# Kernel tuning notes

Hardware: AMD Instinct MI355X
Metric: run time of the kernel (lower is better)

## Reference

```python
import jax, jax.numpy as jnp
import numpy as np

IN_DIM = 128
OUT_DIM = 128
EDGE_DIM = 64
NUM_HEADS = 8
HEAD_DIM = OUT_DIM // NUM_HEADS
N_NODES = 10000
N_EDGES = 320000
LN_EPS = 1e-5


def _gelu(x):
    # torch nn.GELU default is the exact (erf) formulation
    return jax.nn.gelu(x, approximate=False)


def _layernorm(x, g, b):
    mu = jnp.mean(x, axis=-1, keepdims=True)
    var = jnp.var(x, axis=-1, keepdims=True)
    return (x - mu) * jax.lax.rsqrt(var + LN_EPS) * g + b


def setup_inputs() -> dict:
    key = jax.random.key(0)
    ks = jax.random.split(key, 16)

    def lin(k, fan_in, fan_out):
        # torch nn.Linear default init: U(-1/sqrt(fan_in), 1/sqrt(fan_in))
        bound = 1.0 / np.sqrt(fan_in)
        kw, kb = jax.random.split(k)
        w = jax.random.uniform(kw, (fan_in, fan_out), jnp.float32, -bound, bound)
        b = jax.random.uniform(kb, (fan_out,), jnp.float32, -bound, bound)
        return w, b

    node_features = jax.random.normal(ks[0], (N_NODES, IN_DIM), jnp.float32)
    edge_index = jax.random.randint(ks[1], (2, N_EDGES), 0, N_NODES)
    edge_attr = jax.random.normal(ks[2], (N_EDGES, EDGE_DIM), jnp.float32)

    msg_w1, msg_b1 = lin(ks[3], 2 * IN_DIM + EDGE_DIM, OUT_DIM)
    msg_w2, msg_b2 = lin(ks[4], OUT_DIM, OUT_DIM)
    q_w, q_b = lin(ks[5], IN_DIM, OUT_DIM)
    kv_w, kv_b = lin(ks[6], IN_DIM + EDGE_DIM, OUT_DIM)
    out_w1, out_b1 = lin(ks[7], IN_DIM + OUT_DIM, OUT_DIM)
    out_w2, out_b2 = lin(ks[8], OUT_DIM, OUT_DIM)
    ln_g = 1.0 + 0.02 * jax.random.normal(ks[9], (OUT_DIM,), jnp.float32)
    ln_b = 0.02 * jax.random.normal(ks[10], (OUT_DIM,), jnp.float32)

    return dict(node_features=node_features, edge_attr=edge_attr,
                msg_w1=msg_w1, msg_b1=msg_b1, msg_w2=msg_w2, msg_b2=msg_b2,
                q_w=q_w, q_b=q_b, kv_w=kv_w, kv_b=kv_b,
                out_w1=out_w1, out_b1=out_b1, out_w2=out_w2, out_b2=out_b2,
                ln_g=ln_g, ln_b=ln_b, edge_index=edge_index)


def reference(node_features, edge_attr, msg_w1, msg_b1, msg_w2, msg_b2,
              q_w, q_b, kv_w, kv_b, out_w1, out_b1, out_w2, out_b2,
              ln_g, ln_b, edge_index):
    N = node_features.shape[0]
    E = edge_index.shape[1]
    src, dst = edge_index[0], edge_index[1]

    s = node_features[src]                      # [E, Din]
    d = node_features[dst]                      # [E, Din]

    # message MLP
    m_in = jnp.concatenate([s, d, edge_attr], axis=-1)          # [E, 2*Din+De]
    m = _gelu(m_in @ msg_w1 + msg_b1) @ msg_w2 + msg_b2         # [E, Dout]

    # per-edge attention logits
    q = (d @ q_w + q_b).reshape(E, NUM_HEADS, HEAD_DIM)
    kv_in = jnp.concatenate([s, edge_attr], axis=-1)
    kv = (kv_in @ kv_w + kv_b).reshape(E, NUM_HEADS, HEAD_DIM)
    attn = jnp.sum(q * kv, axis=-1) * (HEAD_DIM ** -0.5)        # [E, H]

    # Deterministic version: pick the edge with the largest index per dst node.
    last = jnp.full((N,), -1, dtype=jnp.int32).at[dst].max(
        jnp.arange(E, dtype=jnp.int32))                          # [N]
    attn_full = jnp.where(last[:, None] >= 0,
                          attn[jnp.maximum(last, 0)],
                          -jnp.inf)                              # [N, H]
    # softmax over the NODE axis (dim=0), exactly as the torch code does;
    # -inf rows contribute 0, so using N instead of dst.max()+1 is identical.
    attn_norm = jax.nn.softmax(attn_full, axis=0)[dst]           # [E, H]

    m = (m.reshape(E, NUM_HEADS, HEAD_DIM) * attn_norm[..., None]).reshape(E, OUT_DIM)

    # scatter-add aggregation
    agg = jax.ops.segment_sum(m, dst, num_segments=N)            # [N, Dout]

    h_in = jnp.concatenate([node_features, agg], axis=-1)        # [N, Din+Dout]
    h = _gelu(h_in @ out_w1 + out_b1) @ out_w2 + out_b2          # [N, Dout]

    # res_proj is Identity since in_dim == out_dim; dropout is eval-mode no-op
    return _layernorm(node_features + h, ln_g, ln_b)
```

## Files before the change

kernel.cpp:

```cpp
#include <hip/hip_runtime.h>
#include <hip/hip_bf16.h>

#define NN 10000
#define NE 320000

typedef __bf16 bf16x8 __attribute__((ext_vector_type(8)));
typedef float  f32x4  __attribute__((ext_vector_type(4)));

__device__ __forceinline__ float bf2f(ushort u){
  union { uint i; float f; } c; c.i = ((uint)u) << 16; return c.f;
}
__device__ __forceinline__ ushort f2bf(float f){
  union { float f; uint i; } c; c.f = f;
  uint x = c.i;
  return (ushort)((x + 0x7FFFu + ((x >> 16) & 1u)) >> 16);
}
__device__ __forceinline__ float gelu_erf(float x){
  return 0.5f * x * (1.0f + erff(x * 0.70710678118654752f));
}
__device__ __forceinline__ float gelu_tanh(float x){
  float y = 0.7978845608028654f * (x + 0.044715f * x * x * x);
  float e = __expf(2.f * y);
  float th = 1.f - 2.f / (e + 1.f);
  return 0.5f * x * (1.f + th);
}
__device__ __forceinline__ uint encf(float f){
  uint u = __float_as_uint(f);
  return (u & 0x80000000u) ? ~u : (u | 0x80000000u);
}
__device__ __forceinline__ float decf(uint u){
  return __uint_as_float((u & 0x80000000u) ? (u & 0x7FFFFFFFu) : ~u);
}
#define MFMA16(a,b,c) __builtin_amdgcn_mfma_f32_16x16x32_bf16((a),(b),(c),0,0,0)

__global__ void k_init(const uint* __restrict__ w, int* __restrict__ flag,
                       int* __restrict__ cnt, int* __restrict__ last,
                       uint* __restrict__ Menc, float* __restrict__ S){
  int t = threadIdx.x;
  if (blockIdx.x == 0){
    uint c = 0;
    for (int i = t; i < 4096; i += 256){
      uint v = w[i * 63];
      uint e = (v >> 7) & 0xFF;
      if (e >= 100 && e <= 140) c++;
    }
    __shared__ uint red[256];
    red[t] = c; __syncthreads();
    for (int s = 128; s > 0; s >>= 1){
      if (t < s) red[t] += red[t + s];
      __syncthreads();
    }
    if (t == 0) *flag = (red[0] < 2048) ? 1 : 0;
    return;
  }
  int idx = (blockIdx.x - 1) * 256 + t;
  if (idx < 10000) last[idx] = -1;
  else if (idx < 20000) cnt[idx - 10000] = 0;
  else if (idx < 20008) Menc[idx - 20000] = 0u;
  else if (idx < 20016) S[idx - 20008] = 0.f;
}

__global__ void k_prep(
    const void* NF0, const int* __restrict__ dstI,
    const void* w1, const void* w2, const void* qw, const void* kvw,
    const void* ow1, const void* ow2,
    const void* b1, const void* b2, const void* qb, const void* kvb,
    const void* ob1, const void* ob2, const void* lg, const void* lb,
    int* __restrict__ cnt, int* __restrict__ last,
    ushort* NFc, float* Gagg, ushort* SB, ushort* KVW2,
    ushort* W1aT, ushort* W1bT, ushort* W1cT, ushort* W2T, ushort* QT, ushort* KVT,
    ushort* O1aT, ushort* O1bT, ushort* O2T, const int* flag)
{
  int f = *flag;
  int idx = blockIdx.x * 256 + threadIdx.x;
  if (idx < NE){
    int d = dstI[idx];
    atomicAdd(&cnt[d], 1);
    atomicMax(&last[d], idx);
    return;
  }
  idx -= NE;
  if (idx < 320000){
    if (f){
      float4 v = ((const float4*)NF0)[idx];
      ushort4 o; o.x=f2bf(v.x); o.y=f2bf(v.y); o.z=f2bf(v.z); o.w=f2bf(v.w);
      ((ushort4*)NFc)[idx] = o;
    } else ((ushort4*)NFc)[idx] = ((const ushort4*)NF0)[idx];
    return;
  }
  idx -= 320000;
  if (idx < 320000){ float4 z = {0.f,0.f,0.f,0.f}; ((float4*)Gagg)[idx] = z; return; }
  idx -= 320000;
  if (idx < 1024){
    const void* ps[8] = {b1,b2,qb,kvb,ob1,ob2,lg,lb};
    const void* p = ps[idx >> 7]; int j = idx & 127;
    SB[idx] = f ? f2bf(((const float*)p)[j]) : ((const ushort*)p)[j];
    return;
  }
  idx -= 1024;
  if (idx < 8192){
    KVW2[idx] = f ? f2bf(((const float*)kvw)[16384 + idx]) : ((const ushort*)kvw)[16384 + idx];
    return;
  }
  idx -= 8192;
  if (idx < 16384){ int c=idx>>7,k=idx&127; W1aT[idx] = f? f2bf(((const float*)w1)[k*128+c]) : ((const ushort*)w1)[k*128+c]; return; }
  idx -= 16384;
  if (idx < 16384){ int c=idx>>7,k=idx&127; W1bT[idx] = f? f2bf(((const float*)w1)[(128+k)*128+c]) : ((const ushort*)w1)[(128+k)*128+c]; return; }
  idx -= 16384;
  if (idx < 8192){ int c=idx>>6,k=idx&63;  W1cT[idx] = f? f2bf(((const float*)w1)[(256+k)*128+c]) : ((const ushort*)w1)[(256+k)*128+c]; return; }
  idx -= 8192;
  if (idx < 16384){ int c=idx>>7,k=idx&127; W2T[idx] = f? f2bf(((const float*)w2)[k*128+c]) : ((const ushort*)w2)[k*128+c]; return; }
  idx -= 16384;
  if (idx < 16384){ int c=idx>>7,k=idx&127; QT[idx]  = f? f2bf(((const float*)qw)[k*128+c]) : ((const ushort*)qw)[k*128+c]; return; }
  idx -= 16384;
  if (idx < 16384){ int c=idx>>7,k=idx&127; KVT[idx] = f? f2bf(((const float*)kvw)[k*128+c]) : ((const ushort*)kvw)[k*128+c]; return; }
  idx -= 16384;
  if (idx < 16384){ int c=idx>>7,k=idx&127; O1aT[idx] = f? f2bf(((const float*)ow1)[k*128+c]) : ((const ushort*)ow1)[k*128+c]; return; }
  idx -= 16384;
  if (idx < 16384){ int c=idx>>7,k=idx&127; O1bT[idx] = f? f2bf(((const float*)ow1)[(128+k)*128+c]) : ((const ushort*)ow1)[(128+k)*128+c]; return; }
  idx -= 16384;
  if (idx < 16384){ int c=idx>>7,k=idx&127; O2T[idx] = f? f2bf(((const float*)ow2)[k*128+c]) : ((const ushort*)ow2)[k*128+c]; return; }
}

__global__ __launch_bounds__(1024) void k_scan(const int* __restrict__ cnt,
                                               int* __restrict__ fill){
  __shared__ int sc[1024];
  int t = threadIdx.x;
  int base = t * 10;
  int v[10]; int tot = 0;
  #pragma unroll
  for (int j = 0; j < 10; ++j){
    int idx = base + j;
    v[j] = (idx < NN) ? cnt[idx] : 0;
    tot += v[j];
  }
  sc[t] = tot; __syncthreads();
  for (int off = 1; off < 1024; off <<= 1){
    int x = (t >= off) ? sc[t - off] : 0;
    __syncthreads();
    sc[t] += x;
    __syncthreads();
  }
  int run = sc[t] - tot;
  #pragma unroll
  for (int j = 0; j < 10; ++j){
    int idx = base + j;
    if (idx < NN) fill[idx] = run;
    run += v[j];
  }
}

__global__ __launch_bounds__(256) void k_fillperm(
    const int* __restrict__ srcI, const int* __restrict__ dstI,
    int* __restrict__ fill, int4* __restrict__ sde,
    const ushort* __restrict__ NFc,
    const ushort* __restrict__ W1aT, const ushort* __restrict__ W1bT,
    const ushort* __restrict__ QT,  const ushort* __restrict__ KVT,
    const ushort* __restrict__ SB,
    ushort* __restrict__ PA, ushort* __restrict__ PB,
    ushort* __restrict__ Qb, ushort* __restrict__ KV1)
{
  int t = threadIdx.x;
  if (blockIdx.x >= 1250){
    int l = t & 63, w = t >> 6;
    int m = l & 15, g = l >> 4;
    int row0 = ((int)blockIdx.x - 1250) * 16;
    const ushort* WT = (w==0) ? W1aT : (w==1) ? W1bT : (w==2) ? QT : KVT;
    ushort*       OUT= (w==0) ? PA   : (w==1) ? PB   : (w==2) ? Qb : KV1;
    const f32x4 FZ = {0.f,0.f,0.f,0.f};
    f32x4 acc[8];
    #pragma unroll
    for (int i = 0; i < 8; ++i) acc[i] = FZ;
    int arow = row0 + m;
    #pragma unroll
    for (int ks = 0; ks < 4; ++ks){
      int koff = ks * 32 + g * 8;
      bf16x8 a = *reinterpret_cast<const bf16x8*>(NFc + (size_t)arow * 128 + koff);
      #pragma unroll
      for (int nt = 0; nt < 8; ++nt){
        bf16x8 b = *reinterpret_cast<const bf16x8*>(WT + (size_t)(nt*16+m) * 128 + koff);
        acc[nt] = MFMA16(a, b, acc[nt]);
      }
    }
    #pragma unroll
    for (int nt = 0; nt < 8; ++nt){
      int col = nt * 16 + m;
      float bb = (w==1) ? bf2f(SB[col]) : (w==2) ? bf2f(SB[256+col]) : (w==3) ? bf2f(SB[384+col]) : 0.f;
      #pragma unroll
      for (int r = 0; r < 4; ++r){
        int row = row0 + g * 4 + r;
        OUT[(size_t)row * 128 + col] = f2bf(acc[nt][r] + bb);
      }
    }
    return;
  }
  int e = blockIdx.x * 256 + t;
  int d = dstI[e];
  int s = srcI[e];
  int p = atomicAdd(&fill[d], 1);
  int4 v; v.x = s; v.y = d; v.z = e; v.w = 0;
  sde[p] = v;
}

__global__ __launch_bounds__(256) void k_edgeattn(
    const ushort* __restrict__ PA, const ushort* __restrict__ PB,
    const int4* __restrict__ sde,
    const ushort* __restrict__ W1cT,
    float* __restrict__ Gagg,
    const ushort* __restrict__ Qb, const ushort* __restrict__ KV1,
    const ushort* __restrict__ EAb, const float* __restrict__ EAf,
    const ushort* __restrict__ KVW2,
    const int* __restrict__ srcI, const int* __restrict__ last,
    float* __restrict__ attn, uint* __restrict__ Menc, const int* __restrict__ flag)
{
  __shared__ __align__(16) char Hs[64 * 256];
  __shared__ __align__(16) char EAl[64 * 128];
  __shared__ int sIdx[64], dIdx[64], eIdx[64];
  __shared__ int eN[16], sN[16];
  __shared__ uint lmax[8];
  int t = threadIdx.x;

  if (blockIdx.x >= 5000){
    float (*ea_s)[64] = reinterpret_cast<float(*)[64]>(Hs);
    int n0 = ((int)blockIdx.x - 5000) * 16;
    if (t < 16){
      int e = last[n0 + t];
      eN[t] = e;
      sN[t] = (e >= 0) ? srcI[e] : 0;
    }
    if (t < 8) lmax[t] = 0u;
    __syncthreads();
    int F = *flag;
    for (int i = t; i < 1024; i += 256){
      int nn = i >> 6, k = i & 63;
      int e = eN[nn];
      int ee = (e >= 0) ? e : 0;
      float v = F ? EAf[(size_t)ee * 64 + k] : bf2f(EAb[(size_t)ee * 64 + k]);
      ea_s[nn][k] = (e >= 0) ? v : 0.0f;
    }
    __syncthreads();
    int j = t & 127;
    int half = t >> 7;
    float acc[8];
    #pragma unroll
    for (int i = 0; i < 8; ++i) acc[i] = 0.f;
    for (int k = 0; k < 64; ++k){
      float wv = bf2f(KVW2[(size_t)k * 128 + j]);
      #pragma unroll
      for (int nn = 0; nn < 8; ++nn) acc[nn] += ea_s[half * 8 + nn][k] * wv;
    }
    #pragma unroll
    for (int nn = 0; nn < 8; ++nn){
      int nl = half * 8 + nn;
      int n = n0 + nl;
      int e = eN[nl];
      float kvv = acc[nn] + bf2f(KV1[(size_t)sN[nl] * 128 + j]);
      float qv  = bf2f(Qb[(size_t)n * 128 + j]);
      float p = qv * kvv;
      p += __shfl_xor(p, 1); p += __shfl_xor(p, 2);
      p += __shfl_xor(p, 4); p += __shfl_xor(p, 8);
      if ((j & 15) == 0 && e >= 0){
        float v = p * 0.25f;
        attn[(size_t)n * 8 + (j >> 4)] = v;
        atomicMax(&lmax[j >> 4], encf(v));
      }
    }
    __syncthreads();
    if (t < 8 && lmax[t]) atomicMax(&Menc[t], lmax[t]);
    return;
  }

  int p0 = blockIdx.x * 64;
  int l = t & 63, w = t >> 6;
  int m = l & 15, g = l >> 4;

  if (t < 64){
    int4 v = sde[p0 + t];
    sIdx[t] = v.x; dIdx[t] = v.y; eIdx[t] = v.z;
  }
  __syncthreads();
  int F = *flag;

  {
    int r = t >> 2, q = t & 3;
    int e = eIdx[r];
    int kb = q * 32;
    if (F){
      const float* src = EAf + (size_t)e * 64 + q * 16;
      float4 v0 = *reinterpret_cast<const float4*>(src);
      float4 v1 = *reinterpret_cast<const float4*>(src + 4);
      float4 v2 = *reinterpret_cast<const float4*>(src + 8);
      float4 v3 = *reinterpret_cast<const float4*>(src + 12);
      bf16x8 o0, o1;
      o0[0]=(__bf16)v0.x; o0[1]=(__bf16)v0.y; o0[2]=(__bf16)v0.z; o0[3]=(__bf16)v0.w;
      o0[4]=(__bf16)v1.x; o0[5]=(__bf16)v1.y; o0[6]=(__bf16)v1.z; o0[7]=(__bf16)v1.w;
      o1[0]=(__bf16)v2.x; o1[1]=(__bf16)v2.y; o1[2]=(__bf16)v2.z; o1[3]=(__bf16)v2.w;
      o1[4]=(__bf16)v3.x; o1[5]=(__bf16)v3.y; o1[6]=(__bf16)v3.z; o1[7]=(__bf16)v3.w;
      *reinterpret_cast<bf16x8*>(&EAl[(r * 128 + kb)      ^ ((r & 7) << 4)]) = o0;
      *reinterpret_cast<bf16x8*>(&EAl[(r * 128 + kb + 16) ^ ((r & 7) << 4)]) = o1;
    } else {
      const ushort* src = EAb + (size_t)e * 64 + q * 16;
      *reinterpret_cast<bf16x8*>(&EAl[(r * 128 + kb)      ^ ((r & 7) << 4)]) =
        *reinterpret_cast<const bf16x8*>(src);
      *reinterpret_cast<bf16x8*>(&EAl[(r * 128 + kb + 16) ^ ((r & 7) << 4)]) =
        *reinterpret_cast<const bf16x8*>(src + 8);
    }
    int sr = sIdx[r], dr = dIdx[r];
    #pragma unroll
    for (int j = 0; j < 4; ++j){
      int c8 = q * 4 + j;
      bf16x8 pa = *reinterpret_cast<const bf16x8*>(PA + (size_t)sr * 128 + c8 * 8);
      bf16x8 pb = *reinterpret_cast<const bf16x8*>(PB + (size_t)dr * 128 + c8 * 8);
      bf16x8 ps;
      #pragma unroll
      for (int k = 0; k < 8; ++k) ps[k] = (__bf16)((float)pa[k] + (float)pb[k]);
      int byte = (r * 256 + c8 * 16) ^ ((r & 7) << 4);
      *reinterpret_cast<bf16x8*>(&Hs[byte]) = ps;
    }
  }
  __syncthreads();

  const f32x4 FZ = {0.f,0.f,0.f,0.f};
  f32x4 acc[8];
  #pragma unroll
  for (int i = 0; i < 8; ++i) acc[i] = FZ;

  #pragma unroll
  for (int ks = 0; ks < 2; ++ks){
    int row = w * 16 + m;
    bf16x8 af = *reinterpret_cast<const bf16x8*>(&EAl[(row * 128 + ks * 64 + g * 16) ^ ((row & 7) << 4)]);
    #pragma unroll
    for (int nt = 0; nt < 8; ++nt){
      bf16x8 b = *reinterpret_cast<const bf16x8*>(W1cT + (size_t)(nt * 16 + m) * 64 + ks * 32 + g * 8);
      acc[nt] = MFMA16(af, b, acc[nt]);
    }
  }

  #pragma unroll
  for (int nt = 0; nt < 8; ++nt){
    int col = nt * 16 + m;
    #pragma unroll
    for (int r = 0; r < 4; ++r){
      int row = w * 16 + g * 4 + r;
      int byte = (row * 256 + col * 2) ^ ((row & 7) << 4);
      float x = acc[nt][r] + bf2f(*reinterpret_cast<const ushort*>(&Hs[byte]));
      *reinterpret_cast<ushort*>(&Hs[byte]) = f2bf(gelu_tanh(x));
    }
  }
  __syncthreads();

  {
    int c = t & 127, hh = t >> 7;
    int rS = hh * 32, rE = rS + 32;
    float run = 0.f;
    int cur = dIdx[rS];
    for (int r = rS; r < rE; ++r){
      int d = dIdx[r];
      if (d != cur){
        unsafeAtomicAdd(&Gagg[(size_t)cur * 128 + c], run);
        run = 0.f; cur = d;
      }
      int byte = (r * 256 + c * 2) ^ ((r & 7) << 4);
      run += bf2f(*reinterpret_cast<const ushort*>(&Hs[byte]));
    }
    unsafeAtomicAdd(&Gagg[(size_t)cur * 128 + c], run);
  }
}

__global__ __launch_bounds__(256) void k_asum(
    const float* __restrict__ attn, const int* __restrict__ last,
    const uint* __restrict__ Menc, float* __restrict__ S)
{
  __shared__ float red[256][8];
  int t = threadIdx.x;
  float M[8];
  #pragma unroll
  for (int h = 0; h < 8; ++h) M[h] = decf(Menc[h]);
  float p[8];
  #pragma unroll
  for (int h = 0; h < 8; ++h) p[h] = 0.f;
  for (int n = blockIdx.x * 256 + t; n < NN; n += gridDim.x * 256){
    if (last[n] >= 0){
      #pragma unroll
      for (int h = 0; h < 8; ++h) p[h] += __expf(attn[(size_t)n * 8 + h] - M[h]);
    }
  }
  #pragma unroll
  for (int h = 0; h < 8; ++h) red[t][h] = p[h];
  __syncthreads();
  for (int s = 128; s > 0; s >>= 1){
    if (t < s){
      #pragma unroll
      for (int h = 0; h < 8; ++h) red[t][h] += red[t + s][h];
    }
    __syncthreads();
  }
  if (t < 8) atomicAdd(&S[t], red[0][t]);
}

__global__ __launch_bounds__(256) void k_aggln(
    const float* __restrict__ Gagg, const ushort* __restrict__ W2T,
    const ushort* __restrict__ O1aT, const ushort* __restrict__ O1bT,
    const ushort* __restrict__ O2T,
    const ushort* __restrict__ SB,
    const int* __restrict__ cnt, const int* __restrict__ last,
    const float* __restrict__ attn, const uint* __restrict__ Menc,
    const float* __restrict__ S,
    const ushort* __restrict__ NFc, void* __restrict__ out,
    const int* __restrict__ flag)
{
  __shared__ __align__(16) char Zs[64 * 256];
  int t = threadIdx.x, l = t & 63, w = t >> 6;
  int m = l & 15, g = l >> 4;
  int row0 = blockIdx.x * 64 + w * 16;
  int F = *flag;

  float M[8], Sinv[8];
  #pragma unroll
  for (int h = 0; h < 8; ++h){ M[h] = decf(Menc[h]); Sinv[h] = 1.0f / S[h]; }

  int arow = row0 + m; if (arow >= NN) arow = NN - 1;
  const f32x4 FZ = {0.f,0.f,0.f,0.f};

  f32x4 acc[8];
  #pragma unroll
  for (int i = 0; i < 8; ++i) acc[i] = FZ;
  #pragma unroll
  for (int ks = 0; ks < 4; ++ks){
    const float* gp = Gagg + (size_t)arow * 128 + ks * 32 + g * 8;
    float4 u0 = *reinterpret_cast<const float4*>(gp);
    float4 u1 = *reinterpret_cast<const float4*>(gp + 4);
    float gv[8] = {u0.x,u0.y,u0.z,u0.w,u1.x,u1.y,u1.z,u1.w};
    bf16x8 hi, lo;
    #pragma unroll
    for (int k = 0; k < 8; ++k){
      hi[k] = (__bf16)gv[k];
      lo[k] = (__bf16)(gv[k] - (float)hi[k]);
    }
    #pragma unroll
    for (int nt = 0; nt < 8; ++nt){
      bf16x8 b = *reinterpret_cast<const bf16x8*>(W2T + (size_t)(nt*16+m) * 128 + ks * 32 + g * 8);
      acc[nt] = MFMA16(hi, b, acc[nt]);
      acc[nt] = MFMA16(lo, b, acc[nt]);
    }
  }

  #pragma unroll
  for (int r = 0; r < 4; ++r){
    int row = row0 + g * 4 + r;
    int rr = (row < NN) ? row : NN - 1;
    float cn = (float)cnt[rr];
    int lst = last[rr];
    int Lr = w * 16 + g * 4 + r;
    #pragma unroll
    for (int nt = 0; nt < 8; ++nt){
      int col = nt * 16 + m;
      float aw = (lst >= 0) ? __expf(attn[(size_t)rr * 8 + nt] - M[nt]) * Sinv[nt] : 0.f;
      float z = (acc[nt][r] + cn * bf2f(SB[128 + col])) * aw;
      int byte = (Lr * 256 + col * 2) ^ ((Lr & 7) << 4);
      *reinterpret_cast<ushort*>(&Zs[byte]) = f2bf(z);
    }
  }
  __syncthreads();

  f32x4 acc2[8];
  #pragma unroll
  for (int i = 0; i < 8; ++i) acc2[i] = FZ;
  int La = w * 16 + m;
  #pragma unroll
  for (int ks = 0; ks < 4; ++ks){
    int koff = ks * 32 + g * 8;
    bf16x8 az = *reinterpret_cast<const bf16x8*>(&Zs[(La * 256 + koff * 2) ^ ((La & 7) << 4)]);
    bf16x8 an = *reinterpret_cast<const bf16x8*>(NFc + (size_t)arow * 128 + koff);
    #pragma unroll
    for (int nt = 0; nt < 8; ++nt){
      bf16x8 b1v = *reinterpret_cast<const bf16x8*>(O1bT + (size_t)(nt*16+m) * 128 + koff);
      bf16x8 b2v = *reinterpret_cast<const bf16x8*>(O1aT + (size_t)(nt*16+m) * 128 + koff);
      acc2[nt] = MFMA16(az, b1v, acc2[nt]);
      acc2[nt] = MFMA16(an, b2v, acc2[nt]);
    }
  }
  __syncthreads();

  #pragma unroll
  for (int nt = 0; nt < 8; ++nt){
    int col = nt * 16 + m;
    float bb = bf2f(SB[512 + col]);
    #pragma unroll
    for (int r = 0; r < 4; ++r){
      int Lr = w * 16 + g * 4 + r;
      float v = gelu_erf(acc2[nt][r] + bb);
      int byte = (Lr * 256 + col * 2) ^ ((Lr & 7) << 4);
      *reinterpret_cast<ushort*>(&Zs[byte]) = f2bf(v);
    }
  }
  __syncthreads();

  f32x4 acc3[8];
  #pragma unroll
  for (int i = 0; i < 8; ++i) acc3[i] = FZ;
  #pragma unroll
  for (int ks = 0; ks < 4; ++ks){
    int koff = ks * 32 + g * 8;
    bf16x8 a = *reinterpret_cast<const bf16x8*>(&Zs[(La * 256 + koff * 2) ^ ((La & 7) << 4)]);
    #pragma unroll
    for (int nt = 0; nt < 8; ++nt){
      bf16x8 b = *reinterpret_cast<const bf16x8*>(O2T + (size_t)(nt*16+m) * 128 + koff);
      acc3[nt] = MFMA16(a, b, acc3[nt]);
    }
  }
  #pragma unroll
  for (int r = 0; r < 4; ++r){
    int row = row0 + g * 4 + r;
    bool ok = row < NN;
    int rr = ok ? row : NN - 1;
    float x[8]; float s = 0.f, q = 0.f;
    #pragma unroll
    for (int nt = 0; nt < 8; ++nt){
      int col = nt * 16 + m;
      float xv = acc3[nt][r] + bf2f(SB[640 + col]) + bf2f(NFc[(size_t)rr * 128 + col]);
      x[nt] = xv; s += xv; q += xv * xv;
    }
    #pragma unroll
    for (int msk = 1; msk < 16; msk <<= 1){
      s += __shfl_xor(s, msk);
      q += __shfl_xor(q, msk);
    }
    float mean = s * (1.0f / 128.0f);
    float var  = q * (1.0f / 128.0f) - mean * mean;
    float rs = rsqrtf(var + 1e-5f);
    if (ok){
      #pragma unroll
      for (int nt = 0; nt < 8; ++nt){
        int col = nt * 16 + m;
        float y = (x[nt] - mean) * rs * bf2f(SB[768 + col]) + bf2f(SB[896 + col]);
        if (F) ((float*)out)[(size_t)row * 128 + col] = y;
        else   ((ushort*)out)[(size_t)row * 128 + col] = f2bf(y);
      }
    }
  }
}

extern "C" void kernel_launch(void* const* d_in, const int* in_sizes, int n_in,
                              void* d_out, int out_size, void* d_ws, size_t ws_size,
                              hipStream_t stream)
{
  const void* NF0  = d_in[0];
  const void* EA0  = d_in[1];
  const void* w1   = d_in[2];
  const void* b1   = d_in[3];
  const void* w2   = d_in[4];
  const void* b2   = d_in[5];
  const void* qw   = d_in[6];
  const void* qb   = d_in[7];
  const void* kvw  = d_in[8];
  const void* kvb  = d_in[9];
  const void* ow1  = d_in[10];
  const void* ob1  = d_in[11];
  const void* ow2  = d_in[12];
  const void* ob2  = d_in[13];
  const void* lg   = d_in[14];
  const void* lb   = d_in[15];
  const int*  srcI = (const int*)d_in[16];
  const int*  dstI = srcI + NE;

  char* ws = (char*)d_ws;
  size_t off = 0;
  auto alloc = [&](size_t bytes) -> void* {
    void* p = ws + off;
    off = (off + bytes + 255) & ~(size_t)255;
    return p;
  };
  int*    flag  = (int*)   alloc(4);
  ushort* NFc   = (ushort*)alloc((size_t)NN * 128 * 2);
  ushort* SB    = (ushort*)alloc(8 * 128 * 2);
  ushort* KVW2  = (ushort*)alloc(64 * 128 * 2);
  ushort* W1aT  = (ushort*)alloc(128 * 128 * 2);
  ushort* W1bT  = (ushort*)alloc(128 * 128 * 2);
  ushort* W1cT  = (ushort*)alloc(128 * 64 * 2);
  ushort* W2T   = (ushort*)alloc(128 * 128 * 2);
  ushort* QT    = (ushort*)alloc(128 * 128 * 2);
  ushort* KVT   = (ushort*)alloc(128 * 128 * 2);
  ushort* O1aT  = (ushort*)alloc(128 * 128 * 2);
  ushort* O1bT  = (ushort*)alloc(128 * 128 * 2);
  ushort* O2T   = (ushort*)alloc(128 * 128 * 2);
  int*    last  = (int*)   alloc(NN * 4);
  int*    cnt   = (int*)   alloc(NN * 4);
  int*    fill  = (int*)   alloc(NN * 4);
  int4*   sde   = (int4*)  alloc((size_t)NE * 16);
  float*  attn  = (float*) alloc(NN * 8 * 4);
  uint*   Menc  = (uint*)  alloc(8 * 4);
  float*  S     = (float*) alloc(8 * 4);
  ushort* PA    = (ushort*)alloc((size_t)NN * 128 * 2);
  ushort* PB    = (ushort*)alloc((size_t)NN * 128 * 2);
  ushort* Qb    = (ushort*)alloc((size_t)NN * 128 * 2);
  ushort* KV1   = (ushort*)alloc((size_t)NN * 128 * 2);
  float*  Gagg  = (float*) alloc((size_t)NN * 128 * 4);

  k_init<<<80, 256, 0, stream>>>((const uint*)NF0, flag, cnt, last, Menc, S);
  k_prep<<<4330, 256, 0, stream>>>(NF0, dstI, w1, w2, qw, kvw, ow1, ow2,
                                   b1, b2, qb, kvb, ob1, ob2, lg, lb,
                                   cnt, last, NFc, Gagg, SB, KVW2,
                                   W1aT, W1bT, W1cT, W2T, QT, KVT, O1aT, O1bT, O2T, flag);
  k_scan<<<1, 1024, 0, stream>>>(cnt, fill);
  k_fillperm<<<1875, 256, 0, stream>>>(srcI, dstI, fill, sde,
                                       NFc, W1aT, W1bT, QT, KVT, SB,
                                       PA, PB, Qb, KV1);
  k_edgeattn<<<5625, 256, 0, stream>>>(PA, PB, sde, W1cT, Gagg,
                                       Qb, KV1, (const ushort*)EA0, (const float*)EA0,
                                       KVW2, srcI, last, attn, Menc, flag);
  k_asum<<<40, 256, 0, stream>>>(attn, last, Menc, S);
  k_aggln<<<157, 256, 0, stream>>>(Gagg, W2T, O1aT, O1bT, O2T, SB, cnt, last,
                                   attn, Menc, S, NFc, d_out, flag);
}
```

Baseline: 197.8 us.

## Process two edge tiles per block with prefetch and fold softmax sum into aggln

Each edge-attention block now handles 128 edges as two 64-edge tiles. The second tile's edge attributes and PA/PB rows are loaded into registers while the first tile's MFMA, GELU and scatter run, which is meant to hide gather latency and halve the block count. Separately, the softmax denominator kernel is removed: every k_aggln block now recomputes the per-head exp sum over all nodes itself, dropping one launch and the S buffer. The cost is redundant reduction work in each of the 157 aggln blocks and higher register pressure in the edge kernel.

New measurement: 228.1 us. 1.15x slower.

```diff
diff --git a/kernel.cpp b/kernel.cpp
--- a/kernel.cpp
+++ b/kernel.cpp
@@ -35,7 +35,7 @@
 
 __global__ void k_init(const uint* __restrict__ w, int* __restrict__ flag,
                        int* __restrict__ cnt, int* __restrict__ last,
-                       uint* __restrict__ Menc, float* __restrict__ S){
+                       uint* __restrict__ Menc){
   int t = threadIdx.x;
   if (blockIdx.x == 0){
     uint c = 0;
@@ -57,7 +57,6 @@
   if (idx < 10000) last[idx] = -1;
   else if (idx < 20000) cnt[idx - 10000] = 0;
   else if (idx < 20008) Menc[idx - 20000] = 0u;
-  else if (idx < 20016) S[idx - 20008] = 0.f;
 }
 
 __global__ void k_prep(
@@ -215,14 +214,14 @@
 {
   __shared__ __align__(16) char Hs[64 * 256];
   __shared__ __align__(16) char EAl[64 * 128];
-  __shared__ int sIdx[64], dIdx[64], eIdx[64];
+  __shared__ int sIdx[128], dIdx[128], eIdx[128];
   __shared__ int eN[16], sN[16];
   __shared__ uint lmax[8];
   int t = threadIdx.x;
 
-  if (blockIdx.x >= 5000){
+  if (blockIdx.x >= 2500){
     float (*ea_s)[64] = reinterpret_cast<float(*)[64]>(Hs);
-    int n0 = ((int)blockIdx.x - 5000) * 16;
+    int n0 = ((int)blockIdx.x - 2500) * 16;
     if (t < 16){
       int e = last[n0 + t];
       eN[t] = e;
@@ -270,21 +269,22 @@
     return;
   }
 
-  int p0 = blockIdx.x * 64;
+  int p0 = blockIdx.x * 128;
   int l = t & 63, w = t >> 6;
   int m = l & 15, g = l >> 4;
 
-  if (t < 64){
+  if (t < 128){
     int4 v = sde[p0 + t];
     sIdx[t] = v.x; dIdx[t] = v.y; eIdx[t] = v.z;
   }
   __syncthreads();
   int F = *flag;
 
+  int r = t >> 2, q = t & 3;
+  int kb = q * 32;
+
   {
-    int r = t >> 2, q = t & 3;
     int e = eIdx[r];
-    int kb = q * 32;
     if (F){
       const float* src = EAf + (size_t)e * 64 + q * 16;
       float4 v0 = *reinterpret_cast<const float4*>(src);
@@ -318,13 +318,28 @@
       *reinterpret_cast<bf16x8*>(&Hs[byte]) = ps;
     }
   }
+
+  int e1i = eIdx[64 + r], s1i = sIdx[64 + r], d1i = dIdx[64 + r];
+  float4 ef1a, ef1b, ef1c, ef1d;
+  bf16x8 eb1lo, eb1hi;
+  if (F){
+    const float* src = EAf + (size_t)e1i * 64 + q * 16;
+    ef1a = *reinterpret_cast<const float4*>(src);
+    ef1b = *reinterpret_cast<const float4*>(src + 4);
+    ef1c = *reinterpret_cast<const float4*>(src + 8);
+    ef1d = *reinterpret_cast<const float4*>(src + 12);
+  } else {
+    const ushort* src = EAb + (size_t)e1i * 64 + q * 16;
+    eb1lo = *reinterpret_cast<const bf16x8*>(src);
+    eb1hi = *reinterpret_cast<const bf16x8*>(src + 8);
+  }
   __syncthreads();
 
   const f32x4 FZ = {0.f,0.f,0.f,0.f};
   f32x4 acc[8];
+
   #pragma unroll
   for (int i = 0; i < 8; ++i) acc[i] = FZ;
-
   #pragma unroll
   for (int ks = 0; ks < 2; ++ks){
     int row = w * 16 + m;
@@ -335,17 +350,24 @@
       acc[nt] = MFMA16(af, b, acc[nt]);
     }
   }
-
   #pragma unroll
   for (int nt = 0; nt < 8; ++nt){
     int col = nt * 16 + m;
     #pragma unroll
-    for (int r = 0; r < 4; ++r){
-      int row = w * 16 + g * 4 + r;
+    for (int rr = 0; rr < 4; ++rr){
+      int row = w * 16 + g * 4 + rr;
       int byte = (row * 256 + col * 2) ^ ((row & 7) << 4);
-      float x = acc[nt][r] + bf2f(*reinterpret_cast<const ushort*>(&Hs[byte]));
+      float x = acc[nt][rr] + bf2f(*reinterpret_cast<const ushort*>(&Hs[byte]));
       *reinterpret_cast<ushort*>(&Hs[byte]) = f2bf(gelu_tanh(x));
     }
+  }
+
+  bf16x8 pa1[4], pb1[4];
+  #pragma unroll
+  for (int j = 0; j < 4; ++j){
+    int c8 = q * 4 + j;
+    pa1[j] = *reinterpret_cast<const bf16x8*>(PA + (size_t)s1i * 128 + c8 * 8);
+    pb1[j] = *reinterpret_cast<const bf16x8*>(PB + (size_t)d1i * 128 + c8 * 8);
   }
   __syncthreads();
 
@@ -354,48 +376,85 @@
     int rS = hh * 32, rE = rS + 32;
     float run = 0.f;
     int cur = dIdx[rS];
-    for (int r = rS; r < rE; ++r){
-      int d = dIdx[r];
+    for (int rr = rS; rr < rE; ++rr){
+      int d = dIdx[rr];
       if (d != cur){
         unsafeAtomicAdd(&Gagg[(size_t)cur * 128 + c], run);
         run = 0.f; cur = d;
       }
-      int byte = (r * 256 + c * 2) ^ ((r & 7) << 4);
+      int byte = (rr * 256 + c * 2) ^ ((rr & 7) << 4);
       run += bf2f(*reinterpret_cast<const ushort*>(&Hs[byte]));
     }
     unsafeAtomicAdd(&Gagg[(size_t)cur * 128 + c], run);
   }
-}
-
-__global__ __launch_bounds__(256) void k_asum(
-    const float* __restrict__ attn, const int* __restrict__ last,
-    const uint* __restrict__ Menc, float* __restrict__ S)
-{
-  __shared__ float red[256][8];
-  int t = threadIdx.x;
-  float M[8];
-  #pragma unroll
-  for (int h = 0; h < 8; ++h) M[h] = decf(Menc[h]);
-  float p[8];
-  #pragma unroll
-  for (int h = 0; h < 8; ++h) p[h] = 0.f;
-  for (int n = blockIdx.x * 256 + t; n < NN; n += gridDim.x * 256){
-    if (last[n] >= 0){
-      #pragma unroll
-      for (int h = 0; h < 8; ++h) p[h] += __expf(attn[(size_t)n * 8 + h] - M[h]);
-    }
-  }
-  #pragma unroll
-  for (int h = 0; h < 8; ++h) red[t][h] = p[h];
-  __syncthreads();
-  for (int s = 128; s > 0; s >>= 1){
-    if (t < s){
-      #pragma unroll
-      for (int h = 0; h < 8; ++h) red[t][h] += red[t + s][h];
-    }
-    __syncthreads();
-  }
-  if (t < 8) atomicAdd(&S[t], red[0][t]);
+  __syncthreads();
+
+  {
+    if (F){
+      bf16x8 o0, o1;
+      o0[0]=(__bf16)ef1a.x; o0[1]=(__bf16)ef1a.y; o0[2]=(__bf16)ef1a.z; o0[3]=(__bf16)ef1a.w;
+      o0[4]=(__bf16)ef1b.x; o0[5]=(__bf16)ef1b.y; o0[6]=(__bf16)ef1b.z; o0[7]=(__bf16)ef1b.w;
+      o1[0]=(__bf16)ef1c.x; o1[1]=(__bf16)ef1c.y; o1[2]=(__bf16)ef1c.z; o1[3]=(__bf16)ef1c.w;
+      o1[4]=(__bf16)ef1d.x; o1[5]=(__bf16)ef1d.y; o1[6]=(__bf16)ef1d.z; o1[7]=(__bf16)ef1d.w;
+      *reinterpret_cast<bf16x8*>(&EAl[(r * 128 + kb)      ^ ((r & 7) << 4)]) = o0;
+      *reinterpret_cast<bf16x8*>(&EAl[(r * 128 + kb + 16) ^ ((r & 7) << 4)]) = o1;
+    } else {
+      *reinterpret_cast<bf16x8*>(&EAl[(r * 128 + kb)      ^ ((r & 7) << 4)]) = eb1lo;
+      *reinterpret_cast<bf16x8*>(&EAl[(r * 128 + kb + 16) ^ ((r & 7) << 4)]) = eb1hi;
+    }
+    #pragma unroll
+    for (int j = 0; j < 4; ++j){
+      int c8 = q * 4 + j;
+      bf16x8 ps;
+      #pragma unroll
+      for (int k = 0; k < 8; ++k) ps[k] = (__bf16)((float)pa1[j][k] + (float)pb1[j][k]);
+      int byte = (r * 256 + c8 * 16) ^ ((r & 7) << 4);
+      *reinterpret_cast<bf16x8*>(&Hs[byte]) = ps;
+    }
+  }
+  __syncthreads();
+
+  #pragma unroll
+  for (int i = 0; i < 8; ++i) acc[i] = FZ;
+  #pragma unroll
+  for (int ks = 0; ks < 2; ++ks){
+    int row = w * 16 + m;
+    bf16x8 af = *reinterpret_cast<const bf16x8*>(&EAl[(row * 128 + ks * 64 + g * 16) ^ ((row & 7) << 4)]);
+    #pragma unroll
+    for (int nt = 0; nt < 8; ++nt){
+      bf16x8 b = *reinterpret_cast<const bf16x8*>(W1cT + (size_t)(nt * 16 + m) * 64 + ks * 32 + g * 8);
+      acc[nt] = MFMA16(af, b, acc[nt]);
+    }
+  }
+  #pragma unroll
+  for (int nt = 0; nt < 8; ++nt){
+    int col = nt * 16 + m;
+    #pragma unroll
+    for (int rr = 0; rr < 4; ++rr){
+      int row = w * 16 + g * 4 + rr;
+      int byte = (row * 256 + col * 2) ^ ((row & 7) << 4);
+      float x = acc[nt][rr] + bf2f(*reinterpret_cast<const ushort*>(&Hs[byte]));
+      *reinterpret_cast<ushort*>(&Hs[byte]) = f2bf(gelu_tanh(x));
+    }
+  }
+  __syncthreads();
+
+  {
+    int c = t & 127, hh = t >> 7;
+    int rS = hh * 32, rE = rS + 32;
+    float run = 0.f;
+    int cur = dIdx[64 + rS];
+    for (int rr = rS; rr < rE; ++rr){
+      int d = dIdx[64 + rr];
+      if (d != cur){
+        unsafeAtomicAdd(&Gagg[(size_t)cur * 128 + c], run);
+        run = 0.f; cur = d;
+      }
+      int byte = (rr * 256 + c * 2) ^ ((rr & 7) << 4);
+      run += bf2f(*reinterpret_cast<const ushort*>(&Hs[byte]));
+    }
+    unsafeAtomicAdd(&Gagg[(size_t)cur * 128 + c], run);
+  }
 }
 
 __global__ __launch_bounds__(256) void k_aggln(
@@ -405,7 +464,6 @@
     const ushort* __restrict__ SB,
     const int* __restrict__ cnt, const int* __restrict__ last,
     const float* __restrict__ attn, const uint* __restrict__ Menc,
-    const float* __restrict__ S,
     const ushort* __restrict__ NFc, void* __restrict__ out,
     const int* __restrict__ flag)
 {
@@ -415,9 +473,34 @@
   int row0 = blockIdx.x * 64 + w * 16;
   int F = *flag;
 
-  float M[8], Sinv[8];
-  #pragma unroll
-  for (int h = 0; h < 8; ++h){ M[h] = decf(Menc[h]); Sinv[h] = 1.0f / S[h]; }
+  float M[8];
+  #pragma unroll
+  for (int h = 0; h < 8; ++h) M[h] = decf(Menc[h]);
+
+  float psum[8];
+  #pragma unroll
+  for (int h = 0; h < 8; ++h) psum[h] = 0.f;
+  for (int n = t; n < NN; n += 256){
+    if (last[n] >= 0){
+      #pragma unroll
+      for (int h = 0; h < 8; ++h) psum[h] += __expf(attn[(size_t)n * 8 + h] - M[h]);
+    }
+  }
+  float (*sred)[8] = reinterpret_cast<float(*)[8]>(Zs);
+  #pragma unroll
+  for (int h = 0; h < 8; ++h) sred[t][h] = psum[h];
+  __syncthreads();
+  for (int s = 128; s > 0; s >>= 1){
+    if (t < s){
+      #pragma unroll
+      for (int h = 0; h < 8; ++h) sred[t][h] += sred[t + s][h];
+    }
+    __syncthreads();
+  }
+  float Sinv[8];
+  #pragma unroll
+  for (int h = 0; h < 8; ++h) Sinv[h] = 1.0f / sred[0][h];
+  __syncthreads();
 
   int arow = row0 + m; if (arow >= NN) arow = NN - 1;
   const f32x4 FZ = {0.f,0.f,0.f,0.f};
@@ -590,14 +673,13 @@
   int4*   sde   = (int4*)  alloc((size_t)NE * 16);
   float*  attn  = (float*) alloc(NN * 8 * 4);
   uint*   Menc  = (uint*)  alloc(8 * 4);
-  float*  S     = (float*) alloc(8 * 4);
   ushort* PA    = (ushort*)alloc((size_t)NN * 128 * 2);
   ushort* PB    = (ushort*)alloc((size_t)NN * 128 * 2);
   ushort* Qb    = (ushort*)alloc((size_t)NN * 128 * 2);
   ushort* KV1   = (ushort*)alloc((size_t)NN * 128 * 2);
   float*  Gagg  = (float*) alloc((size_t)NN * 128 * 4);
 
-  k_init<<<80, 256, 0, stream>>>((const uint*)NF0, flag, cnt, last, Menc, S);
+  k_init<<<80, 256, 0, stream>>>((const uint*)NF0, flag, cnt, last, Menc);
   k_prep<<<4330, 256, 0, stream>>>(NF0, dstI, w1, w2, qw, kvw, ow1, ow2,
                                    b1, b2, qb, kvb, ob1, ob2, lg, lb,
                                    cnt, last, NFc, Gagg, SB, KVW2,
@@ -606,10 +688,9 @@
   k_fillperm<<<1875, 256, 0, stream>>>(srcI, dstI, fill, sde,
                                        NFc, W1aT, W1bT, QT, KVT, SB,
                                        PA, PB, Qb, KV1);
-  k_edgeattn<<<5625, 256, 0, stream>>>(PA, PB, sde, W1cT, Gagg,
+  k_edgeattn<<<3125, 256, 0, stream>>>(PA, PB, sde, W1cT, Gagg,
                                        Qb, KV1, (const ushort*)EA0, (const float*)EA0,
                                        KVW2, srcI, last, attn, Menc, flag);
-  k_asum<<<40, 256, 0, stream>>>(attn, last, Menc, S);
   k_aggln<<<157, 256, 0, stream>>>(Gagg, W2T, O1aT, O1bT, O2T, SB, cnt, last,
-                                   attn, Menc, S, NFc, d_out, flag);
-}
+                                   attn, Menc, NFc, d_out, flag);
+}
```
